# Kernel optimization log

Measured on AMD Instinct MI355X. Metric: run time of the kernel, lower is better.

The kernel has to match this reference:

```python
import jax, jax.numpy as jnp
import numpy as np
from jax import lax

B, S, E, H = 8, 1024, 1024, 16
HEAD_DIM = E // H
THRESHOLD = 0.5
NEG_FILL = -1e9


def setup_inputs() -> dict:
    key = jax.random.key(0)
    k0, k1, k2 = jax.random.split(key, 3)
    x = jax.random.normal(k0, (B, S, E), jnp.float32)
    in_proj_w = jax.random.normal(k1, (3 * E, E), jnp.float32) * 0.02
    in_proj_b = jnp.zeros((3 * E,), jnp.float32)
    out_proj_w = jax.random.normal(k2, (E, E), jnp.float32) * 0.02
    out_proj_b = jnp.zeros((E,), jnp.float32)
    return {"x": x, "in_proj_w": in_proj_w, "in_proj_b": in_proj_b,
            "out_proj_w": out_proj_w, "out_proj_b": out_proj_b}


def _mha(x, in_proj_w, in_proj_b, out_proj_w, out_proj_b):
    # PyTorch nn.MultiheadAttention with q=k=v=x, batch_first=True
    qkv = x @ in_proj_w.T + in_proj_b                     # [B,S,3E]
    q, k, v = jnp.split(qkv, 3, axis=-1)                  # each [B,S,E]
    def split_heads(t):
        return t.reshape(B, S, H, HEAD_DIM).transpose(0, 2, 1, 3)  # [B,H,S,d]
    q, k, v = split_heads(q), split_heads(k), split_heads(v)
    scale = 1.0 / np.sqrt(HEAD_DIM).astype(np.float32)
    scores = jnp.einsum('bhqd,bhkd->bhqk', q, k) * scale  # [B,H,S,S]
    w = jax.nn.softmax(scores, axis=-1)
    o = jnp.einsum('bhqk,bhkd->bhqd', w, v)               # [B,H,S,d]
    o = o.transpose(0, 2, 1, 3).reshape(B, S, E)
    attn_output = o @ out_proj_w.T + out_proj_b           # [B,S,E]
    attn_weights = w.mean(axis=1)                         # head-averaged [B,S,S]
    return attn_output, attn_weights


def _cluster(attn_weights):
    # Sequential greedy clustering: scan rows i in order; if row i is not yet
    # visited, its high-attention columns (> THRESHOLD) form cluster i and are
    # marked visited. cluster_id[b, j] = row index of the first cluster that
    # claimed token j, or -1 if never claimed.
    visited0 = jnp.zeros((B, S), dtype=bool)
    cid0 = jnp.full((B, S), -1, dtype=jnp.int32)

    def step(carry, i):
        visited, cid = carry
        process = ~jnp.take(visited, i, axis=1)           # [B] row i unvisited?
        high = jnp.take(attn_weights, i, axis=1) > THRESHOLD  # [B,S]
        claimed = process[:, None] & high                 # [B,S]
        newly = claimed & (~visited)
        cid = jnp.where(newly, jnp.int32(i), cid)
        visited = visited | claimed
        return (visited, cid), None

    (visited, cid), _ = lax.scan(step, (visited0, cid0), jnp.arange(S))
    return cid, visited


def reference(x, in_proj_w, in_proj_b, out_proj_w, out_proj_b):
    attn_output, attn_weights = _mha(x, in_proj_w, in_proj_b, out_proj_w, out_proj_b)
    cluster_ids, covered = _cluster(attn_weights)
    # _generate_image_features: x where token belongs to some cluster, -1e9 else
    clustered_outputs = jnp.where(covered[..., None], x, jnp.float32(NEG_FILL))
    return attn_output, attn_weights, clustered_outputs, cluster_ids
```

## Files before the change

kernel.cpp:

```cpp
#include <hip/hip_runtime.h>
#include <hip/hip_bf16.h>

#define B 8
#define S 1024
#define E 1024
#define H 16

typedef unsigned short u16;
typedef unsigned char u8;
typedef unsigned int u32;
typedef unsigned long long u64;

typedef __attribute__((ext_vector_type(8))) short s16x8;
typedef __attribute__((ext_vector_type(4))) float f32x4;
typedef __attribute__((ext_vector_type(16))) float f32x16;

__device__ __forceinline__ float bf2f(u16 u) {
    union { u32 i; float f; } x; x.i = ((u32)u) << 16; return x.f;
}
__device__ __forceinline__ u16 f2bf(float f) {
    union { float f; u32 i; } x; x.f = f;
    u32 r = x.i + 0x7FFFu + ((x.i >> 16) & 1u);
    return (u16)(r >> 16);
}
__device__ __forceinline__ f32x16 zero16() {
    f32x16 z;
#pragma unroll
    for (int i = 0; i < 16; ++i) z[i] = 0.f;
    return z;
}
__device__ __forceinline__ void gload16(const u16* g, u16* l) {
    __builtin_amdgcn_global_load_lds(
        (const __attribute__((address_space(1))) u32*)g,
        (__attribute__((address_space(3))) u32*)l, 16, 0, 0);
}

__global__ __launch_bounds__(256) void cvt_all(
    const float* __restrict__ x, const float* __restrict__ w0,
    const float* __restrict__ w1, u16* __restrict__ xb,
    u16* __restrict__ wb0, u16* __restrict__ wb1) {
    int i = blockIdx.x * 256 + threadIdx.x;
    const float* src;
    u16* dst;
    int off;
    if (i < 2097152) { src = x; dst = xb; off = i; }
    else if (i < 2883584) { src = w0; dst = wb0; off = i - 2097152; }
    else { src = w1; dst = wb1; off = i - 2883584; }
    float4 v = ((const float4*)src)[off];
    union { u16 u[4]; ushort4 s; } p;
    p.u[0] = f2bf(v.x); p.u[1] = f2bf(v.y);
    p.u[2] = f2bf(v.z); p.u[3] = f2bf(v.w);
    ((ushort4*)dst)[off] = p.s;
}

template <int MODE>
__global__ __launch_bounds__(256) void mfma_gemm(
    const u16* __restrict__ A, const u16* __restrict__ W,
    const float* __restrict__ bias, u16* __restrict__ qb, u16* __restrict__ kb,
    u16* __restrict__ vt, float* __restrict__ outf) {
    __shared__ __align__(16) u16 As[128 * 64];
    __shared__ __align__(16) u16 Bs[128 * 64];
    const int t = threadIdx.x;
    const int lane = t & 63;
    const int w = t >> 6;
    const int tot = (int)(gridDim.x * gridDim.y);
    const int lin = (int)(blockIdx.y * gridDim.x + blockIdx.x);
    const int cpx = tot >> 3;
    const int sw = (lin & 7) * cpx + (lin >> 3);
    const int m0 = (sw & 63) * 128;
    const int n0 = (sw >> 6) * 128;
    const int wm = w >> 1, wn = w & 1;
    const int l15 = lane & 15, l4 = lane >> 4;
    const int lr = lane >> 3;
    const int lc = (lane & 7) * 8;

    f32x4 acc[4][4];
#pragma unroll
    for (int i = 0; i < 4; ++i)
#pragma unroll
        for (int j = 0; j < 4; ++j) acc[i][j] = {0.f, 0.f, 0.f, 0.f};

    for (int k0 = 0; k0 < 1024; k0 += 64) {
        __syncthreads();
#pragma unroll
        for (int jj = 0; jj < 4; ++jj) {
            int j = w * 4 + jj;
            gload16(A + (size_t)(m0 + j * 8 + lr) * 1024 + k0 + lc, As + j * 512);
            gload16(W + (size_t)(n0 + j * 8 + lr) * 1024 + k0 + lc, Bs + j * 512);
        }
        __syncthreads();
#pragma unroll
        for (int ks = 0; ks < 2; ++ks) {
            s16x8 af[4], bf[4];
#pragma unroll
            for (int i = 0; i < 4; ++i)
                af[i] = *(const s16x8*)(As + (wm * 64 + i * 16 + l15) * 64 + ks * 32 + l4 * 8);
#pragma unroll
            for (int j = 0; j < 4; ++j)
                bf[j] = *(const s16x8*)(Bs + (wn * 64 + j * 16 + l15) * 64 + ks * 32 + l4 * 8);
#pragma unroll
            for (int i = 0; i < 4; ++i)
#pragma unroll
                for (int j = 0; j < 4; ++j)
                    acc[i][j] = __builtin_amdgcn_mfma_f32_16x16x32_bf16(
                        af[i], bf[j], acc[i][j], 0, 0, 0);
        }
    }

    if (MODE == 0) {
#pragma unroll
        for (int j = 0; j < 4; ++j) {
            int n = n0 + wn * 64 + j * 16 + l15;
            float bn = bias[n];
            int seg = n >> 10;
            int e = n & 1023;
            int hh = e >> 6, d = e & 63;
            float sc = (seg == 0) ? 0.18033688011f : 1.0f;
#pragma unroll
            for (int i = 0; i < 4; ++i) {
                int mbase = m0 + wm * 64 + i * 16 + l4 * 4;
                int bb = mbase >> 10, sb = mbase & 1023;
                if (seg == 2) {
                    union { u16 u[4]; ushort4 s; } p;
#pragma unroll
                    for (int rr = 0; rr < 4; ++rr) p.u[rr] = f2bf(acc[i][j][rr] + bn);
                    *(ushort4*)(vt + ((size_t)(bb * 16 + hh) * 64 + d) * 1024 + sb) = p.s;
                } else {
                    u16* dst = (seg == 0) ? qb : kb;
#pragma unroll
                    for (int rr = 0; rr < 4; ++rr)
                        dst[((size_t)(bb * 16 + hh) * 1024 + sb + rr) * 64 + d] =
                            f2bf((acc[i][j][rr] + bn) * sc);
                }
            }
        }
    } else {
#pragma unroll
        for (int j = 0; j < 4; ++j) {
            int n = n0 + wn * 64 + j * 16 + l15;
            float bn = bias[n];
#pragma unroll
            for (int i = 0; i < 4; ++i) {
                int mbase = m0 + wm * 64 + i * 16 + l4 * 4;
#pragma unroll
                for (int rr = 0; rr < 4; ++rr)
                    outf[(size_t)(mbase + rr) * 1024 + n] = acc[i][j][rr] + bn;
            }
        }
    }
}

template <int BASE>
__device__ __forceinline__ s16x8 build_pa(f32x16 e) {
    u32 a, bv, c, d;
    asm("v_cvt_pk_bf16_f32 %0, %1, %2" : "=v"(a) : "v"(e[BASE + 0]), "v"(e[BASE + 1]));
    asm("v_cvt_pk_bf16_f32 %0, %1, %2" : "=v"(bv) : "v"(e[BASE + 2]), "v"(e[BASE + 3]));
    asm("v_cvt_pk_bf16_f32 %0, %1, %2" : "=v"(c) : "v"(e[BASE + 4]), "v"(e[BASE + 5]));
    asm("v_cvt_pk_bf16_f32 %0, %1, %2" : "=v"(d) : "v"(e[BASE + 6]), "v"(e[BASE + 7]));
    asm("v_permlane32_swap_b32 %0, %1" : "+v"(a), "+v"(c));
    asm("v_permlane32_swap_b32 %0, %1" : "+v"(bv), "+v"(d));
    union { u32 w[4]; s16x8 v; } u;
    u.w[0] = a; u.w[1] = bv; u.w[2] = c; u.w[3] = d;
    return u.v;
}
__device__ __forceinline__ float pair_max(float v) {
    float a_ = v, b_ = v;
    asm("v_permlane32_swap_b32 %0, %1" : "+v"(a_), "+v"(b_));
    return fmaxf(a_, b_);
}
__device__ __forceinline__ float pair_sum(float v) {
    float a_ = v, b_ = v;
    asm("v_permlane32_swap_b32 %0, %1" : "+v"(a_), "+v"(b_));
    return a_ + b_;
}
__device__ __forceinline__ u32 pair_or(u32 v) {
    u32 a_ = v, b_ = v;
    asm("v_permlane32_swap_b32 %0, %1" : "+v"(a_), "+v"(b_));
    return a_ | b_;
}

__global__ __launch_bounds__(256, 4) void attn_flash(
    const u16* __restrict__ qg, const u16* __restrict__ kg,
    const u16* __restrict__ vtg, u16* __restrict__ og,
    float* __restrict__ stats) {
    __shared__ __align__(16) u16 bufK[2][64 * 64];
    __shared__ __align__(16) u16 bufV[2][64 * 64];
    const int t = threadIdx.x;
    const int lane = t & 63;
    const int w = t >> 6;
    const int task = ((blockIdx.x & 7) << 7) | (blockIdx.x >> 3);
    const int b = task >> 7;
    const int h = (task >> 3) & 15;
    const int qg_ = task & 7;
    const int q = lane & 31;
    const int hi = lane >> 5;
    const int q0 = qg_ * 128 + w * 32;
    const size_t hb = (size_t)(b * 16 + h) << 16;

    const int lr = lane >> 3;
    const int lc = ((lane & 7) ^ lr) * 8;
    const int swz = (q & 7) << 4;

#define STAGE(tt, bb)                                                          \
    do {                                                                       \
        _Pragma("unroll") for (int jj = 0; jj < 2; ++jj) {                     \
            int j = w * 2 + jj;                                                \
            gload16(kg + hb + (size_t)((tt) * 64 + j * 8 + lr) * 64 + lc,      \
                    bufK[bb] + j * 512);                                       \
            gload16(vtg + hb + (size_t)(j * 8 + lr) * 1024 + (tt) * 64 + lc,   \
                    bufV[bb] + j * 512);                                       \
        }                                                                      \
    } while (0)

    s16x8 qf[4];
#pragma unroll
    for (int s = 0; s < 4; ++s)
        qf[s] = *(const s16x8*)(qg + hb + (size_t)(q0 + q) * 64 + s * 16 + hi * 8);

    f32x16 oLo = zero16(), oHi = zero16();
    float m = -1e30f, l = 0.f;

    STAGE(0, 0);
    __syncthreads();
    int cur = 0;

    for (int tile = 0; tile < 16; ++tile) {
        if (tile < 15) STAGE(tile + 1, cur ^ 1);
        const u16* bK = bufK[cur];
        const u16* bV = bufV[cur];
#pragma unroll
        for (int kk = 0; kk < 64; kk += 32) {
            s16x8 ka[4];
#pragma unroll
            for (int s = 0; s < 4; ++s)
                ka[s] = *(const s16x8*)((const u8*)bK +
                        ((((kk + q) << 7) + (s << 5) + (hi << 4)) ^ swz));
            f32x16 s_ = zero16();
#pragma unroll
            for (int s = 0; s < 4; ++s)
                s_ = __builtin_amdgcn_mfma_f32_32x32x16_bf16(ka[s], qf[s], s_, 0, 0, 0);
            float m0 = fmaxf(fmaxf(s_[0], s_[4]), fmaxf(s_[8], s_[12]));
            float m1 = fmaxf(fmaxf(s_[1], s_[5]), fmaxf(s_[9], s_[13]));
            float m2 = fmaxf(fmaxf(s_[2], s_[6]), fmaxf(s_[10], s_[14]));
            float m3 = fmaxf(fmaxf(s_[3], s_[7]), fmaxf(s_[11], s_[15]));
            float pmax = pair_max(fmaxf(fmaxf(m0, m1), fmaxf(m2, m3)));
            if (__any(pmax > m + 11.5f)) {
                float mn = fmaxf(m, pmax);
                float r = exp2f(m - mn);
                m = mn;
                l *= r;
                oLo = oLo * r;
                oHi = oHi * r;
            }
            float s0 = 0.f, s1 = 0.f, s2 = 0.f, s3 = 0.f;
#pragma unroll
            for (int i = 0; i < 16; i += 4) {
                s_[i + 0] = exp2f(s_[i + 0] - m);
                s_[i + 1] = exp2f(s_[i + 1] - m);
                s_[i + 2] = exp2f(s_[i + 2] - m);
                s_[i + 3] = exp2f(s_[i + 3] - m);
                s0 += s_[i + 0]; s1 += s_[i + 1]; s2 += s_[i + 2]; s3 += s_[i + 3];
            }
            l += pair_sum((s0 + s1) + (s2 + s3));
            s16x8 p0 = build_pa<0>(s_), p1 = build_pa<8>(s_);
            s16x8 vLo0 = *(const s16x8*)((const u8*)bV +
                         (((q << 7) + (kk << 1) + (hi << 4)) ^ swz));
            s16x8 vLo1 = *(const s16x8*)((const u8*)bV +
                         (((q << 7) + (kk << 1) + 32 + (hi << 4)) ^ swz));
            s16x8 vHi0 = *(const s16x8*)((const u8*)bV +
                         ((((q + 32) << 7) + (kk << 1) + (hi << 4)) ^ swz));
            s16x8 vHi1 = *(const s16x8*)((const u8*)bV +
                         ((((q + 32) << 7) + (kk << 1) + 32 + (hi << 4)) ^ swz));
            oLo = __builtin_amdgcn_mfma_f32_32x32x16_bf16(vLo0, p0, oLo, 0, 0, 0);
            oLo = __builtin_amdgcn_mfma_f32_32x32x16_bf16(vLo1, p1, oLo, 0, 0, 0);
            oHi = __builtin_amdgcn_mfma_f32_32x32x16_bf16(vHi0, p0, oHi, 0, 0, 0);
            oHi = __builtin_amdgcn_mfma_f32_32x32x16_bf16(vHi1, p1, oHi, 0, 0, 0);
        }
        __syncthreads();
        cur ^= 1;
    }
#undef STAGE
    float inv = 1.0f / l;
    oLo = oLo * inv;
    oHi = oHi * inv;
    u16* orow = og + (size_t)(b * 1024 + q0 + q) * 1024 + h * 64;
#pragma unroll
    for (int rg = 0; rg < 4; ++rg) {
        union { u16 u[4]; u64 v; } pk;
#pragma unroll
        for (int j = 0; j < 4; ++j) pk.u[j] = f2bf(oLo[4 * rg + j]);
        *(u64*)(orow + 8 * rg + 4 * hi) = pk.v;
#pragma unroll
        for (int j = 0; j < 4; ++j) pk.u[j] = f2bf(oHi[4 * rg + j]);
        *(u64*)(orow + 32 + 4 * hi + 8 * rg) = pk.v;
    }
    if (hi == 0)
        stats[(size_t)(b * 16 + h) * 1024 + q0 + q] = m + 4.0f + log2f(l);
}

__global__ __launch_bounds__(256, 3) void attn_aw(
    const u16* __restrict__ qg, const u16* __restrict__ kg,
    const float* __restrict__ stats, float* __restrict__ aw,
    u64* __restrict__ maskg) {
    __shared__ __align__(16) u16 bufK[2][64 * 64];
    __shared__ __align__(16) u16 bufQ[2][128 * 64];
    const int t = threadIdx.x;
    const int lane = t & 63;
    const int w = t >> 6;
    const int sw = ((blockIdx.x & 7) << 7) | (blockIdx.x >> 3);
    const int b = sw >> 7;
    const int ks = (sw >> 3) & 15;
    const int qg_ = sw & 7;
    const int q = lane & 31;
    const int hi = lane >> 5;
    const int q0 = qg_ * 128;
    const int qr = w * 32 + q;
    const int kbase = ks * 64;

    const int lr = lane >> 3;
    const int lc = ((lane & 7) ^ lr) * 8;
    const int swz = (q & 7) << 4;

#define STAGEAW(hh, bb)                                                        \
    do {                                                                       \
        const size_t hbs = (size_t)(b * 16 + (hh)) << 16;                      \
        _Pragma("unroll") for (int jj = 0; jj < 2; ++jj) {                     \
            int j = w * 2 + jj;                                                \
            gload16(kg + hbs + (size_t)(kbase + j * 8 + lr) * 64 + lc,         \
                    bufK[bb] + j * 512);                                       \
        }                                                                      \
        _Pragma("unroll") for (int jj = 0; jj < 4; ++jj) {                     \
            int j = w * 4 + jj;                                                \
            gload16(qg + hbs + (size_t)(q0 + j * 8 + lr) * 64 + lc,            \
                    bufQ[bb] + j * 512);                                       \
        }                                                                      \
    } while (0)

    f32x16 awA = zero16(), awB = zero16();

    STAGEAW(0, 0);
    __syncthreads();
    int cur = 0;

    for (int h = 0; h < 16; ++h) {
        if (h < 15) STAGEAW(h + 1, cur ^ 1);
        const u16* bK = bufK[cur];
        const u16* bQ = bufQ[cur];
        s16x8 qf[4], kA[4], kB[4];
#pragma unroll
        for (int s = 0; s < 4; ++s) {
            qf[s] = *(const s16x8*)((const u8*)bQ +
                    (((qr << 7) + (s << 5) + (hi << 4)) ^ swz));
            kA[s] = *(const s16x8*)((const u8*)bK +
                    (((q << 7) + (s << 5) + (hi << 4)) ^ swz));
            kB[s] = *(const s16x8*)((const u8*)bK +
                    ((((q + 32) << 7) + (s << 5) + (hi << 4)) ^ swz));
        }
        float C = stats[(size_t)(b * 16 + h) * 1024 + q0 + qr];
        f32x16 sA = zero16(), sB = zero16();
#pragma unroll
        for (int s = 0; s < 4; ++s) {
            sA = __builtin_amdgcn_mfma_f32_32x32x16_bf16(kA[s], qf[s], sA, 0, 0, 0);
            sB = __builtin_amdgcn_mfma_f32_32x32x16_bf16(kB[s], qf[s], sB, 0, 0, 0);
        }
#pragma unroll
        for (int i = 0; i < 16; ++i) {
            awA[i] += exp2f(sA[i] - C);
            awB[i] += exp2f(sB[i] - C);
        }
        __syncthreads();
        cur ^= 1;
    }
#undef STAGEAW
    float* awrow = aw + (size_t)(b * 1024 + q0 + qr) * 1024 + kbase;
#pragma unroll
    for (int rg = 0; rg < 4; ++rg) {
        *(float4*)(awrow + 8 * rg + 4 * hi) =
            make_float4(awA[4 * rg + 0], awA[4 * rg + 1], awA[4 * rg + 2], awA[4 * rg + 3]);
        *(float4*)(awrow + 32 + 8 * rg + 4 * hi) =
            make_float4(awB[4 * rg + 0], awB[4 * rg + 1], awB[4 * rg + 2], awB[4 * rg + 3]);
    }
    u32 lo = 0, hi32 = 0;
#pragma unroll
    for (int r = 0; r < 16; ++r) {
        int k = (r & 3) + 8 * (r >> 2) + 4 * hi;
        lo |= (awA[r] > 0.5f) ? (1u << k) : 0u;
        hi32 |= (awB[r] > 0.5f) ? (1u << k) : 0u;
    }
    lo = pair_or(lo);
    hi32 = pair_or(hi32);
    if (hi == 0)
        maskg[(size_t)(b * 1024 + q0 + qr) * 16 + ks] = ((u64)hi32 << 32) | (u64)lo;
}

__global__ __launch_bounds__(256) void cluster_kernel(
    const u64* __restrict__ maskg, float* __restrict__ cid, u64* __restrict__ cov) {
    __shared__ u64 mask[16384];
    __shared__ u16 rows[1024];
    const int t = threadIdx.x;
    const int b = blockIdx.x;
#pragma unroll
    for (int i = 0; i < 64; ++i)
        mask[t + 256 * i] = maskg[(size_t)b * 16384 + t + 256 * i];
#pragma unroll
    for (int i = 0; i < 4; ++i) cid[b * S + t + 256 * i] = -1.0f;
    __syncthreads();
    if (t < 64) {
        int nr = 0;
        for (int it = 0; it < 16; ++it) {
            int row = it * 64 + t;
            const u64* mp = mask + row * 16;
            u64 orv = 0;
#pragma unroll
            for (int j = 0; j < 16; ++j) orv |= mp[j];
            u64 bal = __ballot(orv != 0ULL);
            int pre = __popcll(bal & ((1ULL << t) - 1ULL));
            if (orv != 0ULL) rows[nr + pre] = (u16)row;
            nr += __popcll(bal);
        }
        u64 vis = 0;
        for (int idx = 0; idx < nr; ++idx) {
            int i = rows[idx];
            u64 viw = __shfl(vis, i >> 6);
            bool proc = ((viw >> (i & 63)) & 1ULL) == 0ULL;
            u64 cl = (proc && t < 16) ? mask[i * 16 + t] : 0ULL;
            u64 newly = cl & ~vis;
            vis |= cl;
            while (newly) {
                int bit = __ffsll((long long)newly) - 1;
                cid[b * S + t * 64 + bit] = (float)i;
                newly &= newly - 1;
            }
        }
        if (t < 16) cov[b * 16 + t] = vis;
    }
}

__global__ __launch_bounds__(256) void clustered_kernel(
    const float* __restrict__ x, const u64* __restrict__ cov,
    float* __restrict__ out2) {
    const size_t n4 = (size_t)B * S * E / 4;
    size_t idx = (size_t)blockIdx.x * 256 + threadIdx.x;
    const float4 neg = make_float4(-1e9f, -1e9f, -1e9f, -1e9f);
    for (; idx < n4; idx += (size_t)gridDim.x * 256) {
        size_t tok = idx >> 8;
        int bb = (int)(tok >> 10), s = (int)(tok & 1023);
        u64 m = cov[bb * 16 + (s >> 6)];
        bool c = ((m >> (s & 63)) & 1ULL) != 0ULL;
        float4 v = ((const float4*)x)[idx];
        ((float4*)out2)[idx] = c ? v : neg;
    }
}

extern "C" void kernel_launch(void* const* d_in, const int* in_sizes, int n_in,
                              void* d_out, int out_size, void* d_ws, size_t ws_size,
                              hipStream_t stream) {
    const float* x = (const float*)d_in[0];
    const float* w_in = (const float*)d_in[1];
    const float* b_in = (const float*)d_in[2];
    const float* w_out = (const float*)d_in[3];
    const float* b_out = (const float*)d_in[4];

    float* out0 = (float*)d_out;
    float* out1 = out0 + 8388608;
    float* out2 = out1 + 8388608;
    float* out3 = out2 + 8388608;

    u16* q_bf = (u16*)out0;
    u16* vt_bf = q_bf + 8388608;
    u16* xb = (u16*)out1;
    u16* k_bf = (u16*)out2;
    u16* wb0 = k_bf + 8388608;
    u16* wb1 = wb0 + 3145728;
    float* statsF = (float*)(k_bf + 12582912);
    u16* o_bf = (u16*)d_ws;
    u64* maskg = (u64*)((char*)d_ws + (size_t)(16u << 20));
    u64* cov = (u64*)((char*)d_ws + (size_t)(17u << 20));

    cvt_all<<<12288, 256, 0, stream>>>(x, w_in, w_out, xb, wb0, wb1);

    mfma_gemm<0><<<dim3(64, 24), 256, 0, stream>>>(xb, wb0, b_in, q_bf, k_bf,
                                                   vt_bf, nullptr);
    attn_flash<<<1024, 256, 0, stream>>>(q_bf, k_bf, vt_bf, o_bf, statsF);
    attn_aw<<<1024, 256, 0, stream>>>(q_bf, k_bf, statsF, out1, maskg);
    mfma_gemm<1><<<dim3(64, 8), 256, 0, stream>>>(o_bf, wb1, b_out, nullptr,
                                                  nullptr, nullptr, out0);

    cluster_kernel<<<8, 256, 0, stream>>>(maskg, out3, cov);
    clustered_kernel<<<2048, 256, 0, stream>>>(x, cov, out2);
}
```

Measured before the change: 267.2 us.

## Swizzle GEMM LDS tiles and stage QKV epilogue through shared memory

The shared-memory A/B tiles get an XOR swizzle on both the global-to-LDS copy and the fragment reads, to cut bank conflicts on the MFMA operand loads. The QKV projection epilogue now writes the tile into LDS first, then stores Q/K/V (including the transposed V) with coalesced 16-byte global writes instead of scattered 2-byte stores. This adds extra barriers and an LDS round trip per tile.

```diff
diff --git a/kernel.cpp b/kernel.cpp
--- a/kernel.cpp
+++ b/kernel.cpp
@@ -58,8 +58,9 @@
     const u16* __restrict__ A, const u16* __restrict__ W,
     const float* __restrict__ bias, u16* __restrict__ qb, u16* __restrict__ kb,
     u16* __restrict__ vt, float* __restrict__ outf) {
-    __shared__ __align__(16) u16 As[128 * 64];
-    __shared__ __align__(16) u16 Bs[128 * 64];
+    __shared__ __align__(16) u16 smem[16384];
+    u16* As = smem;
+    u16* Bs = smem + 8192;
     const int t = threadIdx.x;
     const int lane = t & 63;
     const int w = t >> 6;
@@ -72,7 +73,7 @@
     const int wm = w >> 1, wn = w & 1;
     const int l15 = lane & 15, l4 = lane >> 4;
     const int lr = lane >> 3;
-    const int lc = (lane & 7) * 8;
+    const int lc = ((lane & 7) ^ lr) * 8;
 
     f32x4 acc[4][4];
 #pragma unroll
@@ -93,11 +94,17 @@
         for (int ks = 0; ks < 2; ++ks) {
             s16x8 af[4], bf[4];
 #pragma unroll
-            for (int i = 0; i < 4; ++i)
-                af[i] = *(const s16x8*)(As + (wm * 64 + i * 16 + l15) * 64 + ks * 32 + l4 * 8);
-#pragma unroll
-            for (int j = 0; j < 4; ++j)
-                bf[j] = *(const s16x8*)(Bs + (wn * 64 + j * 16 + l15) * 64 + ks * 32 + l4 * 8);
+            for (int i = 0; i < 4; ++i) {
+                int row = wm * 64 + i * 16 + l15;
+                af[i] = *(const s16x8*)((const u8*)As +
+                        (((row << 7) + (ks << 6) + (l4 << 4)) ^ ((row & 7) << 4)));
+            }
+#pragma unroll
+            for (int j = 0; j < 4; ++j) {
+                int row = wn * 64 + j * 16 + l15;
+                bf[j] = *(const s16x8*)((const u8*)Bs +
+                        (((row << 7) + (ks << 6) + (l4 << 4)) ^ ((row & 7) << 4)));
+            }
 #pragma unroll
             for (int i = 0; i < 4; ++i)
 #pragma unroll
@@ -108,30 +115,66 @@
     }
 
     if (MODE == 0) {
-#pragma unroll
-        for (int j = 0; j < 4; ++j) {
-            int n = n0 + wn * 64 + j * 16 + l15;
-            float bn = bias[n];
-            int seg = n >> 10;
-            int e = n & 1023;
-            int hh = e >> 6, d = e & 63;
-            float sc = (seg == 0) ? 0.18033688011f : 1.0f;
-#pragma unroll
-            for (int i = 0; i < 4; ++i) {
-                int mbase = m0 + wm * 64 + i * 16 + l4 * 4;
-                int bb = mbase >> 10, sb = mbase & 1023;
-                if (seg == 2) {
-                    union { u16 u[4]; ushort4 s; } p;
-#pragma unroll
-                    for (int rr = 0; rr < 4; ++rr) p.u[rr] = f2bf(acc[i][j][rr] + bn);
-                    *(ushort4*)(vt + ((size_t)(bb * 16 + hh) * 64 + d) * 1024 + sb) = p.s;
-                } else {
-                    u16* dst = (seg == 0) ? qb : kb;
+        __syncthreads();
+        u16* Cs = smem;
+        const int seg = n0 >> 10;
+        const int bb = m0 >> 10;
+        const int ms = m0 & 1023;
+        if (seg < 2) {
+            const float sc = (seg == 0) ? 0.18033688011f : 1.0f;
+#pragma unroll
+            for (int j = 0; j < 4; ++j) {
+                int nl = wn * 64 + j * 16 + l15;
+                float bn = bias[n0 + nl];
+#pragma unroll
+                for (int i = 0; i < 4; ++i) {
+                    int ml = wm * 64 + i * 16 + l4 * 4;
 #pragma unroll
                     for (int rr = 0; rr < 4; ++rr)
-                        dst[((size_t)(bb * 16 + hh) * 1024 + sb + rr) * 64 + d] =
-                            f2bf((acc[i][j][rr] + bn) * sc);
+                        Cs[(ml + rr) * 128 + nl] = f2bf((acc[i][j][rr] + bn) * sc);
                 }
+            }
+            __syncthreads();
+            u16* dst0 = (seg == 0) ? qb : kb;
+#pragma unroll
+            for (int it = 0; it < 8; ++it) {
+                int flat = it * 256 + t;
+                int ml = flat >> 4;
+                int g = (flat >> 3) & 1;
+                int c8 = flat & 7;
+                int hh = ((n0 + g * 64) & 1023) >> 6;
+                u16* dst = dst0 + (((size_t)(bb * 16 + hh) * 1024 + ms + ml) << 6) + c8 * 8;
+                *(uint4*)dst = *(const uint4*)(Cs + ml * 128 + g * 64 + c8 * 8);
+            }
+        } else {
+#pragma unroll
+            for (int j = 0; j < 4; ++j) {
+                int nl = wn * 64 + j * 16 + l15;
+                float bn = bias[n0 + nl];
+                int sz = (nl & 7) << 4;
+#pragma unroll
+                for (int i = 0; i < 4; ++i) {
+                    int ml = wm * 64 + i * 16 + l4 * 4;
+#pragma unroll
+                    for (int rr = 0; rr < 4; ++rr) {
+                        int bl = (ml + rr) << 1;
+                        *(u16*)((u8*)Cs + (nl << 8) + (bl ^ sz)) =
+                            f2bf(acc[i][j][rr] + bn);
+                    }
+                }
+            }
+            __syncthreads();
+#pragma unroll
+            for (int it = 0; it < 8; ++it) {
+                int flat = it * 256 + t;
+                int nl = flat >> 4;
+                int c = flat & 15;
+                int n = n0 + nl;
+                int hh = (n & 1023) >> 6;
+                int d = n & 63;
+                u16* dst = vt + ((size_t)(bb * 16 + hh) * 64 + d) * 1024 + ms + c * 8;
+                *(uint4*)dst = *(const uint4*)((u8*)Cs + (nl << 8) +
+                                               ((c << 4) ^ ((nl & 7) << 4)));
             }
         }
     } else {
```

Result: faster. 252.4 us (-5.6%).
